# Kernel tuning notes

Measured on AMD Instinct MI355X. Metric: run time of the kernel, lower is better.

The kernel has to match this reference:

```python
import jax, jax.numpy as jnp
import numpy as np

B, N, D, H = 2, 2048, 512, 8
HD = D // H
EPS = 1e-5


def layernorm(x, g, b):
    m = jnp.mean(x, axis=-1, keepdims=True)
    v = jnp.var(x, axis=-1, keepdims=True)
    return (x - m) * jax.lax.rsqrt(v + EPS) * g + b


def setup_inputs() -> dict:
    key = jax.random.key(0)
    ks = jax.random.split(key, 16)
    s = 1.0 / np.sqrt(D)
    def lin(k, din, dout):
        k1, k2 = jax.random.split(k)
        return (jax.random.uniform(k1, (din, dout), jnp.float32, -s, s),
                jax.random.uniform(k2, (dout,), jnp.float32, -s, s))
    Wq, bq = lin(ks[0], D, D)
    Wk, bk = lin(ks[1], D, D)
    Wv, bv = lin(ks[2], D, D)
    Wo, bo = lin(ks[3], D, D)
    W1, b1 = lin(ks[4], D, 2 * D)
    W2, b2 = lin(ks[5], 2 * D, D)
    return {
        'y': jax.random.normal(ks[6], (B, N, D), jnp.float32),
        'Wq': Wq, 'bq': bq, 'Wk': Wk, 'bk': bk, 'Wv': Wv, 'bv': bv,
        'Wo': Wo, 'bo': bo,
        'ln1_g': jnp.ones((D,)), 'ln1_b': jnp.zeros((D,)),
        'ln2_g': jnp.ones((D,)), 'ln2_b': jnp.zeros((D,)),
        'W1': W1, 'b1': b1, 'W2': W2, 'b2': b2,
    }


def reference(y, Wq, bq, Wk, bk, Wv, bv, Wo, bo, ln1_g, ln1_b, ln2_g, ln2_b, W1, b1, W2, b2):
    x = layernorm(y, ln1_g, ln1_b)
    def heads(W, b):
        return (x @ W + b).reshape(B, N, H, HD).transpose(0, 2, 1, 3)  # bhnc
    q = heads(Wq, bq)
    k = heads(Wk, bk)
    v = heads(Wv, bv)
    score = jax.nn.softmax(jnp.einsum('bhic,bhjc->bhij', q, k) / np.sqrt(HD), axis=-1)
    r = jnp.einsum('bhij,bhjc->bhic', score, v)
    r = r.transpose(0, 2, 1, 3).reshape(B, N, D) @ Wo + bo
    y = y + r
    h = layernorm(y, ln2_g, ln2_b)
    h = jax.nn.gelu(h @ W1 + b1, approximate=False) @ W2 + b2
    return y + h
```

## Files before the change

kernel.cpp:

```cpp
#include <hip/hip_runtime.h>

#define DEVI __device__ __forceinline__

typedef unsigned short u16;
typedef unsigned int   u32;
typedef unsigned long long u64;
typedef float  f32x4  __attribute__((ext_vector_type(4)));
typedef __bf16 bf16x8 __attribute__((ext_vector_type(8)));

union FragU { bf16x8 b; u64 u[2]; __bf16 e[8]; };

DEVI u16 f2b(float x) { __bf16 t = (__bf16)x; return __builtin_bit_cast(u16, t); }

DEVI float exp2a(float x) { float r; asm("v_exp_f32 %0, %1" : "=v"(r) : "v"(x)); return r; }

DEVI void gload16(const void* g, void* l) {
  __builtin_amdgcn_global_load_lds((const __attribute__((address_space(1))) u32*)g,
                                   (__attribute__((address_space(3))) u32*)l, 16, 0, 0);
}

DEVI int kperm(int b) {
  return (b & 0x47) | ((b & 0x18) << 1) | ((b & 0x20) >> 2);
}
DEVI int swzo(int row, int b) {
  const int p = kperm(b);
  return ((((p >> 4) ^ row) & 7) << 4) | (p & 15);
}
DEVI FragU ldfrag(const char* base, int row, int g) {
  return *reinterpret_cast<const FragU*>(base + row * 128 + (((g ^ (row & 7)) << 4)));
}
DEVI size_t gaddr(int row, int kbyte, int rowbytes) {
  return (size_t)row * rowbytes + (size_t)((kbyte & ~127) + swzo(row, kbyte & 127));
}

__global__ __launch_bounds__(256)
void prep(const float* __restrict__ Wq, const float* __restrict__ Wk,
          const float* __restrict__ Wv, const float* __restrict__ Wo,
          const float* __restrict__ W1, const float* __restrict__ W2,
          u16* __restrict__ wqkvT, u16* __restrict__ woT,
          u16* __restrict__ w1T, u16* __restrict__ w2T,
          const float* __restrict__ y, const float* __restrict__ ln1g,
          const float* __restrict__ ln1b, char* __restrict__ xb) {
  const int id = blockIdx.x;
  if (id < 2048) {
    __shared__ float tile[32][33];
    const float* src; u16* dst; int K, N, bx, by;
    if (id < 1024) {
      const int m = id >> 8, t = id & 255;
      K = 512; N = 512; bx = t & 15; by = t >> 4;
      src = (m == 0) ? Wq : (m == 1) ? Wk : (m == 2) ? Wv : Wo;
      dst = (m == 3) ? woT : wqkvT + m * 512 * 512;
    } else if (id < 1536) {
      const int t = id - 1024; K = 512; N = 1024; bx = t & 31; by = t >> 5;
      src = W1; dst = w1T;
    } else {
      const int t = id - 1536; K = 1024; N = 512; bx = t & 15; by = t >> 4;
      src = W2; dst = w2T;
    }
    const int tx = threadIdx.x & 31, ty = threadIdx.x >> 5;
#pragma unroll
    for (int i = 0; i < 4; ++i)
      tile[ty + i * 8][tx] = src[(size_t)(by * 32 + ty + i * 8) * N + bx * 32 + tx];
    __syncthreads();
    const int nl = threadIdx.x >> 3, kq = threadIdx.x & 7;
    const int n = bx * 32 + nl;
    const int kg = by * 32 + kq * 4;
    union { ushort4 s; u64 q; } pk;
    pk.s.x = f2b(tile[kq * 4 + 0][nl]);
    pk.s.y = f2b(tile[kq * 4 + 1][nl]);
    pk.s.z = f2b(tile[kq * 4 + 2][nl]);
    pk.s.w = f2b(tile[kq * 4 + 3][nl]);
    *(u64*)((char*)dst + gaddr(n, 2 * kg, 2 * K)) = pk.q;
  } else {
    const int row = id - 2048;
    const int t = threadIdx.x;
    const float2 v = ((const float2*)(y + (size_t)row * 512))[t];
    float s1 = v.x + v.y, s2 = v.x * v.x + v.y * v.y;
#pragma unroll
    for (int off = 32; off; off >>= 1) { s1 += __shfl_xor(s1, off); s2 += __shfl_xor(s2, off); }
    __shared__ float a1[4], a2[4];
    const int w = t >> 6;
    if ((t & 63) == 0) { a1[w] = s1; a2[w] = s2; }
    __syncthreads();
    s1 = a1[0] + a1[1] + a1[2] + a1[3];
    s2 = a2[0] + a2[1] + a2[2] + a2[3];
    const float mean = s1 * (1.f / 512.f);
    const float var = s2 * (1.f / 512.f) - mean * mean;
    const float rstd = rsqrtf(var + 1e-5f);
    const float2 gg = ((const float2*)ln1g)[t];
    const float2 bb = ((const float2*)ln1b)[t];
    const u16 o0 = f2b((v.x - mean) * rstd * gg.x + bb.x);
    const u16 o1 = f2b((v.y - mean) * rstd * gg.y + bb.y);
    *(u32*)(xb + gaddr(row, 4 * t, 1024)) = (u32)o0 | ((u32)o1 << 16);
  }
}

__global__ __launch_bounds__(256)
void ln_bf16(const float* __restrict__ x, const float* __restrict__ g,
             const float* __restrict__ b, char* __restrict__ out) {
  const int row = blockIdx.x;
  const int t = threadIdx.x;
  const float2 v = ((const float2*)(x + (size_t)row * 512))[t];
  float s1 = v.x + v.y, s2 = v.x * v.x + v.y * v.y;
#pragma unroll
  for (int off = 32; off; off >>= 1) { s1 += __shfl_xor(s1, off); s2 += __shfl_xor(s2, off); }
  __shared__ float a1[4], a2[4];
  const int w = t >> 6;
  if ((t & 63) == 0) { a1[w] = s1; a2[w] = s2; }
  __syncthreads();
  s1 = a1[0] + a1[1] + a1[2] + a1[3];
  s2 = a2[0] + a2[1] + a2[2] + a2[3];
  const float mean = s1 * (1.f / 512.f);
  const float var = s2 * (1.f / 512.f) - mean * mean;
  const float rstd = rsqrtf(var + 1e-5f);
  const float2 gg = ((const float2*)g)[t];
  const float2 bb = ((const float2*)b)[t];
  const u16 o0 = f2b((v.x - mean) * rstd * gg.x + bb.x);
  const u16 o1 = f2b((v.y - mean) * rstd * gg.y + bb.y);
  *(u32*)(out + gaddr(row, 4 * t, 1024)) = (u32)o0 | ((u32)o1 << 16);
}

enum { EPI_QKV = 0, EPI_RES = 1, EPI_GELU = 2 };

template <int EPI, int WM, int WN, int AM, int AN>
__global__ __launch_bounds__(WM * WN * 64)
void gemm_bf16(const char* __restrict__ A, const char* __restrict__ Bt, int N, int K,
               const float* __restrict__ bias,
               const float* __restrict__ bq, const float* __restrict__ bk,
               const float* __restrict__ bv,
               const float* __restrict__ res, float* __restrict__ outF,
               char* __restrict__ outB,
               u16* __restrict__ qo, char* __restrict__ ko, char* __restrict__ vo) {
  constexpr int NW = WM * WN;
  constexpr int TM = WM * AM * 16, TN = WN * AN * 16;
  constexpr int NCHA = TM / 8, NCHB = TN / 8, NCH = NCHA + NCHB;
  constexpr int CPW = NCH / NW;
  static_assert(CPW * NW == NCH, "chunk split");
  __shared__ __align__(16) char sA[2][TM * 128];
  __shared__ __align__(16) char sB[2][TN * 128];
  const int tid = threadIdx.x;
  const int l = tid & 63, w = tid >> 6;
  const int tm = blockIdx.x, tn = blockIdx.y;
  const int wr = w / WN, wc = w % WN;
  const int u = l >> 4, r16 = l & 15;
  const int lrow = l >> 3, lgr = l & 7;
  f32x4 acc[AM][AN] = {};
  const size_t KB = (size_t)K * 2;
  const char* Ab = A + (size_t)(tm * TM) * KB;
  const char* Bb = Bt + (size_t)(tn * TN) * KB;
  const int nkt = K >> 6;
  auto stage = [&](int buf, int kt) {
#pragma unroll
    for (int i = 0; i < CPW; ++i) {
      const int c = w * CPW + i;
      if (c < NCHA) {
        gload16(Ab + (size_t)(c * 8 + lrow) * KB + (size_t)kt * 128 + (lgr << 4),
                sA[buf] + c * 1024);
      } else {
        const int c2 = c - NCHA;
        gload16(Bb + (size_t)(c2 * 8 + lrow) * KB + (size_t)kt * 128 + (lgr << 4),
                sB[buf] + c2 * 1024);
      }
    }
  };
  stage(0, 0);
  int cur = 0;
  for (int kt = 0; kt < nkt; ++kt) {
    __syncthreads();
    if (kt + 1 < nkt) stage(cur ^ 1, kt + 1);
    __builtin_amdgcn_s_setprio(1);
#pragma unroll
    for (int ks = 0; ks < 2; ++ks) {
      FragU af[AM], bfr[AN];
      const int g = ks * 4 + u;
#pragma unroll
      for (int i = 0; i < AM; ++i)
        af[i] = ldfrag(sA[cur], wr * (AM * 16) + i * 16 + r16, g);
#pragma unroll
      for (int i = 0; i < AN; ++i)
        bfr[i] = ldfrag(sB[cur], wc * (AN * 16) + i * 16 + r16, g);
#pragma unroll
      for (int mi = 0; mi < AM; ++mi)
#pragma unroll
        for (int ni = 0; ni < AN; ++ni)
          acc[mi][ni] = __builtin_amdgcn_mfma_f32_16x16x32_bf16(af[mi].b, bfr[ni].b,
                                                                acc[mi][ni], 0, 0, 0);
    }
    __builtin_amdgcn_s_setprio(0);
    cur ^= 1;
  }
  const int row0 = tm * TM + wr * (AM * 16) + (u << 2);
  const int col0 = tn * TN + wc * (AN * 16) + r16;
#pragma unroll
  for (int mi = 0; mi < AM; ++mi) {
#pragma unroll
    for (int ni = 0; ni < AN; ++ni) {
      const int col = col0 + ni * 16;
      if (EPI == EPI_RES) {
#pragma unroll
        for (int r = 0; r < 4; ++r) {
          const int row = row0 + mi * 16 + r;
          outF[(size_t)row * N + col] = acc[mi][ni][r] + bias[col] + res[(size_t)row * N + col];
        }
      } else if (EPI == EPI_GELU) {
#pragma unroll
        for (int r = 0; r < 4; ++r) {
          const int row = row0 + mi * 16 + r;
          const float x = acc[mi][ni][r] + bias[col];
          *(u16*)(outB + gaddr(row, 2 * col, 2 * N)) =
              f2b(0.5f * x * (1.f + erff(x * 0.70710678118f)));
        }
      } else {
        const int which = col >> 9, cc = col & 511;
        const int h = cc >> 6, hd = cc & 63;
        if (which == 2) {
          const int rowa = row0 + mi * 16;
          const int bb2 = rowa >> 11, nt0 = rowa & 2047;
          const int bh = bb2 * 8 + h;
          const float bvv = bv[cc];
          union { ushort4 s; u64 q; } pk;
          pk.s.x = f2b(acc[mi][ni][0] + bvv);
          pk.s.y = f2b(acc[mi][ni][1] + bvv);
          pk.s.z = f2b(acc[mi][ni][2] + bvv);
          pk.s.w = f2b(acc[mi][ni][3] + bvv);
          *(u64*)(vo + (size_t)bh * 262144 + (size_t)(nt0 >> 6) * 8192 +
                  gaddr(hd, 2 * (nt0 & 63), 128)) = pk.q;
        } else {
#pragma unroll
          for (int r = 0; r < 4; ++r) {
            const int row = row0 + mi * 16 + r;
            const int bb2 = row >> 11, nt = row & 2047;
            const int bh = bb2 * 8 + h;
            if (which == 0)
              qo[((size_t)bh * 2048 + nt) * 64 + hd] = f2b((acc[mi][ni][r] + bq[cc]) * 0.18033688f);
            else
              *(u16*)(ko + (size_t)bh * 262144 + (size_t)(nt >> 6) * 8192 +
                      gaddr(nt & 63, 2 * hd, 128)) = f2b(acc[mi][ni][r] + bk[cc]);
          }
        }
      }
    }
  }
}

__global__ __launch_bounds__(256)
void attn_k(const u16* __restrict__ q, const char* __restrict__ kswz,
            const char* __restrict__ vswz, char* __restrict__ r_out) {
  __shared__ __align__(16) char sK[2][2][8192];
  __shared__ __align__(16) char sV[2][2][8192];
  const int tid = threadIdx.x;
  const int l = tid & 63, w = tid >> 6;
  const int kvh = w & 1, qw = w >> 1;
  const int bh = blockIdx.x, qt = blockIdx.y;
  const int u = l >> 4, r16 = l & 15;
  const char* kp = kswz + (size_t)bh * 262144;
  const char* vp = vswz + (size_t)bh * 262144;
  auto stage = [&](int buf, int t) {
#pragma unroll
    for (int c = 0; c < 4; ++c) {
      gload16(kp + (size_t)t * 8192 + qw * 4096 + c * 1024 + l * 16,
              sK[kvh][buf] + qw * 4096 + c * 1024);
      gload16(vp + (size_t)t * 8192 + qw * 4096 + c * 1024 + l * 16,
              sV[kvh][buf] + qw * 4096 + c * 1024);
    }
  };
  stage(0, kvh * 16);
  FragU qf[2][2], ones;
  {
#pragma unroll
    for (int f = 0; f < 2; ++f) {
      const u16* qr = q + (size_t)bh * (2048 * 64) +
                      (size_t)(qt * 64 + qw * 32 + f * 16 + r16) * 64 + (u << 2);
      qf[f][0].u[0] = *(const u64*)qr;        qf[f][0].u[1] = *(const u64*)(qr + 16);
      qf[f][1].u[0] = *(const u64*)(qr + 32); qf[f][1].u[1] = *(const u64*)(qr + 48);
    }
    ones.u[0] = 0x3F803F803F803F80ull;
    ones.u[1] = 0x3F803F803F803F80ull;
  }
  f32x4 o[4][2] = {};
  f32x4 lacc[2] = {};
  int cur = 0;
  for (int i = 0; i < 16; ++i) {
    __syncthreads();
    if (i < 15) stage(cur ^ 1, kvh * 16 + i + 1);
    f32x4 st[4][2] = {};
    __builtin_amdgcn_s_setprio(1);
#pragma unroll
    for (int ks = 0; ks < 2; ++ks) {
      const int g = ks * 4 + u;
#pragma unroll
      for (int mi = 0; mi < 4; ++mi) {
        const FragU kf = ldfrag(sK[kvh][cur], mi * 16 + r16, g);
#pragma unroll
        for (int f = 0; f < 2; ++f)
          st[mi][f] = __builtin_amdgcn_mfma_f32_16x16x32_bf16(kf.b, qf[f][ks].b,
                                                              st[mi][f], 0, 0, 0);
      }
    }
    __builtin_amdgcn_s_setprio(0);
#pragma unroll
    for (int mi = 0; mi < 4; ++mi)
#pragma unroll
      for (int f = 0; f < 2; ++f)
#pragma unroll
        for (int r = 0; r < 4; ++r) st[mi][f][r] = exp2a(st[mi][f][r]);
    FragU pb[2][2];
#pragma unroll
    for (int f = 0; f < 2; ++f)
#pragma unroll
      for (int ks = 0; ks < 2; ++ks)
#pragma unroll
        for (int j = 0; j < 4; ++j) {
          pb[f][ks].e[j]     = (__bf16)st[2 * ks][f][j];
          pb[f][ks].e[j + 4] = (__bf16)st[2 * ks + 1][f][j];
        }
    __builtin_amdgcn_s_setprio(1);
#pragma unroll
    for (int ks = 0; ks < 2; ++ks) {
      const int g = ks * 4 + u;
#pragma unroll
      for (int f = 0; f < 2; ++f)
        lacc[f] = __builtin_amdgcn_mfma_f32_16x16x32_bf16(ones.b, pb[f][ks].b, lacc[f], 0, 0, 0);
#pragma unroll
      for (int mo = 0; mo < 4; ++mo) {
        const FragU vf = ldfrag(sV[kvh][cur], mo * 16 + r16, g);
#pragma unroll
        for (int f = 0; f < 2; ++f)
          o[mo][f] = __builtin_amdgcn_mfma_f32_16x16x32_bf16(vf.b, pb[f][ks].b,
                                                             o[mo][f], 0, 0, 0);
      }
    }
    __builtin_amdgcn_s_setprio(0);
    cur ^= 1;
  }
  __syncthreads();
  float* scrO = (float*)&sK[0][0][0];
  float* scrL = (float*)&sV[0][0][0];
  if (kvh == 1) {
    if (u == 0)
#pragma unroll
      for (int f = 0; f < 2; ++f) scrL[qw * 32 + f * 16 + r16] = lacc[f][0];
#pragma unroll
    for (int mo = 0; mo < 4; ++mo)
#pragma unroll
      for (int f = 0; f < 2; ++f)
#pragma unroll
        for (int r = 0; r < 4; ++r)
          scrO[qw * 2048 + (mo * 16 + u * 4 + r) * 32 + f * 16 + r16] = o[mo][f][r];
  }
  __syncthreads();
  if (kvh == 0) {
    const int h = bh & 7;
#pragma unroll
    for (int f = 0; f < 2; ++f) {
      const float linv = 1.f / (lacc[f][0] + scrL[qw * 32 + f * 16 + r16]);
      const int tok = (bh >> 3) * 2048 + qt * 64 + qw * 32 + f * 16 + r16;
#pragma unroll
      for (int mo = 0; mo < 4; ++mo) {
        union { ushort4 s; u64 qq; } pk;
        float vv[4];
#pragma unroll
        for (int r = 0; r < 4; ++r)
          vv[r] = (o[mo][f][r] + scrO[qw * 2048 + (mo * 16 + u * 4 + r) * 32 + f * 16 + r16]) * linv;
        pk.s.x = f2b(vv[0]); pk.s.y = f2b(vv[1]); pk.s.z = f2b(vv[2]); pk.s.w = f2b(vv[3]);
        *(u64*)(r_out + (size_t)tok * 1024 + h * 128 + swzo(tok, mo * 32 + (u << 3))) = pk.qq;
      }
    }
  }
}

extern "C" void kernel_launch(void* const* d_in, const int* in_sizes, int n_in,
                              void* d_out, int out_size, void* d_ws, size_t ws_size,
                              hipStream_t stream) {
  const float* y    = (const float*)d_in[0];
  const float* Wq   = (const float*)d_in[1];
  const float* bq   = (const float*)d_in[2];
  const float* Wk   = (const float*)d_in[3];
  const float* bk   = (const float*)d_in[4];
  const float* Wv   = (const float*)d_in[5];
  const float* bv   = (const float*)d_in[6];
  const float* Wo   = (const float*)d_in[7];
  const float* bo   = (const float*)d_in[8];
  const float* ln1g = (const float*)d_in[9];
  const float* ln1b = (const float*)d_in[10];
  const float* ln2g = (const float*)d_in[11];
  const float* ln2b = (const float*)d_in[12];
  const float* W1   = (const float*)d_in[13];
  const float* b1   = (const float*)d_in[14];
  const float* W2   = (const float*)d_in[15];
  const float* b2   = (const float*)d_in[16];
  float* out = (float*)d_out;
  char* ws = (char*)d_ws;
  char* xb    = ws;
  u16*  qb    = (u16*)(ws + (4u << 20));
  char* kswz  = ws + (8u << 20);
  char* vswz  = ws + (12u << 20);
  char* rb    = ws + (16u << 20);
  char* g1b   = ws + (20u << 20);
  u16* wqkvT  = (u16*)(ws + (28u << 20));
  u16* woT    = wqkvT + 1536 * 512;
  u16* w1T    = woT + 512 * 512;
  u16* w2T    = w1T + 1024 * 512;

  prep<<<6144, 256, 0, stream>>>(Wq, Wk, Wv, Wo, W1, W2, wqkvT, woT, w1T, w2T,
                                 y, ln1g, ln1b, xb);
  gemm_bf16<EPI_QKV, 2, 2, 4, 2><<<dim3(32, 24), 256, 0, stream>>>(
      xb, (const char*)wqkvT, 1536, 512, nullptr, bq, bk, bv,
      nullptr, nullptr, nullptr, qb, kswz, vswz);
  attn_k<<<dim3(16, 32), 256, 0, stream>>>(qb, kswz, vswz, rb);
  gemm_bf16<EPI_RES, 2, 2, 2, 2><<<dim3(64, 8), 256, 0, stream>>>(
      rb, (const char*)woT, 512, 512, bo, nullptr, nullptr, nullptr,
      y, out, nullptr, nullptr, nullptr, nullptr);
  ln_bf16<<<4096, 256, 0, stream>>>(out, ln2g, ln2b, xb);
  gemm_bf16<EPI_GELU, 2, 2, 4, 4><<<dim3(32, 8), 256, 0, stream>>>(
      xb, (const char*)w1T, 1024, 512, b1, nullptr, nullptr, nullptr,
      nullptr, nullptr, g1b, nullptr, nullptr, nullptr);
  gemm_bf16<EPI_RES, 2, 2, 2, 2><<<dim3(64, 8), 256, 0, stream>>>(
      g1b, (const char*)w2T, 512, 1024, b2, nullptr, nullptr, nullptr,
      out, out, nullptr, nullptr, nullptr, nullptr);
}
```

Before: 98.40 us.

## Split attention KV sequence four ways across 512-thread blocks with 32-key tiles

```diff
diff --git a/kernel.cpp b/kernel.cpp
--- a/kernel.cpp
+++ b/kernel.cpp
@@ -28,6 +28,9 @@
 }
 DEVI FragU ldfrag(const char* base, int row, int g) {
   return *reinterpret_cast<const FragU*>(base + row * 128 + (((g ^ (row & 7)) << 4)));
+}
+DEVI FragU ldfrag64(const char* base, int row, int g) {
+  return *reinterpret_cast<const FragU*>(base + row * 64 + (((g ^ (row & 3)) << 4)));
 }
 DEVI size_t gaddr(int row, int kbyte, int rowbytes) {
   return (size_t)row * rowbytes + (size_t)((kbyte & ~127) + swzo(row, kbyte & 127));
@@ -223,8 +226,9 @@
           pk.s.y = f2b(acc[mi][ni][1] + bvv);
           pk.s.z = f2b(acc[mi][ni][2] + bvv);
           pk.s.w = f2b(acc[mi][ni][3] + bvv);
-          *(u64*)(vo + (size_t)bh * 262144 + (size_t)(nt0 >> 6) * 8192 +
-                  gaddr(hd, 2 * (nt0 & 63), 128)) = pk.q;
+          const int kl = nt0 & 31;
+          const int off64 = ((((kl >> 2) & 3) ^ (hd & 3)) << 4) | (((kl >> 4) & 1) << 3);
+          *(u64*)(vo + (size_t)bh * 262144 + (size_t)(nt0 >> 5) * 4096 + hd * 64 + off64) = pk.q;
         } else {
 #pragma unroll
           for (int r = 0; r < 4; ++r) {
@@ -243,28 +247,30 @@
   }
 }
 
-__global__ __launch_bounds__(256)
+__global__ __launch_bounds__(512, 4)
 void attn_k(const u16* __restrict__ q, const char* __restrict__ kswz,
             const char* __restrict__ vswz, char* __restrict__ r_out) {
-  __shared__ __align__(16) char sK[2][2][8192];
-  __shared__ __align__(16) char sV[2][2][8192];
+  __shared__ __align__(16) char smem[65536];
+  char (*sK)[2][4096] = (char(*)[2][4096])smem;
+  char (*sV)[2][4096] = (char(*)[2][4096])(smem + 32768);
   const int tid = threadIdx.x;
   const int l = tid & 63, w = tid >> 6;
-  const int kvh = w & 1, qw = w >> 1;
+  const int kvh = w & 3, qw = w >> 2;
   const int bh = blockIdx.x, qt = blockIdx.y;
   const int u = l >> 4, r16 = l & 15;
   const char* kp = kswz + (size_t)bh * 262144;
   const char* vp = vswz + (size_t)bh * 262144;
-  auto stage = [&](int buf, int t) {
-#pragma unroll
-    for (int c = 0; c < 4; ++c) {
-      gload16(kp + (size_t)t * 8192 + qw * 4096 + c * 1024 + l * 16,
-              sK[kvh][buf] + qw * 4096 + c * 1024);
-      gload16(vp + (size_t)t * 8192 + qw * 4096 + c * 1024 + l * 16,
-              sV[kvh][buf] + qw * 4096 + c * 1024);
+  auto stage = [&](int buf, int i) {
+    const int t32 = kvh * 16 + i;
+    const size_t koff = (size_t)(t32 >> 1) * 8192 + (size_t)(t32 & 1) * 4096;
+    const size_t voff = (size_t)t32 * 4096;
+#pragma unroll
+    for (int c = 0; c < 2; ++c) {
+      gload16(kp + koff + qw * 2048 + c * 1024 + l * 16, sK[kvh][buf] + qw * 2048 + c * 1024);
+      gload16(vp + voff + qw * 2048 + c * 1024 + l * 16, sV[kvh][buf] + qw * 2048 + c * 1024);
     }
   };
-  stage(0, kvh * 16);
+  stage(0, 0);
   FragU qf[2][2], ones;
   {
 #pragma unroll
@@ -282,14 +288,14 @@
   int cur = 0;
   for (int i = 0; i < 16; ++i) {
     __syncthreads();
-    if (i < 15) stage(cur ^ 1, kvh * 16 + i + 1);
-    f32x4 st[4][2] = {};
+    if (i < 15) stage(cur ^ 1, i + 1);
+    f32x4 st[2][2] = {};
     __builtin_amdgcn_s_setprio(1);
 #pragma unroll
     for (int ks = 0; ks < 2; ++ks) {
       const int g = ks * 4 + u;
 #pragma unroll
-      for (int mi = 0; mi < 4; ++mi) {
+      for (int mi = 0; mi < 2; ++mi) {
         const FragU kf = ldfrag(sK[kvh][cur], mi * 16 + r16, g);
 #pragma unroll
         for (int f = 0; f < 2; ++f)
@@ -299,69 +305,73 @@
     }
     __builtin_amdgcn_s_setprio(0);
 #pragma unroll
-    for (int mi = 0; mi < 4; ++mi)
+    for (int mi = 0; mi < 2; ++mi)
 #pragma unroll
       for (int f = 0; f < 2; ++f)
 #pragma unroll
         for (int r = 0; r < 4; ++r) st[mi][f][r] = exp2a(st[mi][f][r]);
-    FragU pb[2][2];
+    FragU pb[2];
 #pragma unroll
     for (int f = 0; f < 2; ++f)
 #pragma unroll
-      for (int ks = 0; ks < 2; ++ks)
-#pragma unroll
-        for (int j = 0; j < 4; ++j) {
-          pb[f][ks].e[j]     = (__bf16)st[2 * ks][f][j];
-          pb[f][ks].e[j + 4] = (__bf16)st[2 * ks + 1][f][j];
-        }
+      for (int j = 0; j < 4; ++j) {
+        pb[f].e[j]     = (__bf16)st[0][f][j];
+        pb[f].e[j + 4] = (__bf16)st[1][f][j];
+      }
     __builtin_amdgcn_s_setprio(1);
 #pragma unroll
-    for (int ks = 0; ks < 2; ++ks) {
-      const int g = ks * 4 + u;
+    for (int f = 0; f < 2; ++f)
+      lacc[f] = __builtin_amdgcn_mfma_f32_16x16x32_bf16(ones.b, pb[f].b, lacc[f], 0, 0, 0);
+#pragma unroll
+    for (int mo = 0; mo < 4; ++mo) {
+      const FragU vf = ldfrag64(sV[kvh][cur], mo * 16 + r16, u);
 #pragma unroll
       for (int f = 0; f < 2; ++f)
-        lacc[f] = __builtin_amdgcn_mfma_f32_16x16x32_bf16(ones.b, pb[f][ks].b, lacc[f], 0, 0, 0);
-#pragma unroll
-      for (int mo = 0; mo < 4; ++mo) {
-        const FragU vf = ldfrag(sV[kvh][cur], mo * 16 + r16, g);
-#pragma unroll
-        for (int f = 0; f < 2; ++f)
-          o[mo][f] = __builtin_amdgcn_mfma_f32_16x16x32_bf16(vf.b, pb[f][ks].b,
-                                                             o[mo][f], 0, 0, 0);
-      }
+        o[mo][f] = __builtin_amdgcn_mfma_f32_16x16x32_bf16(vf.b, pb[f].b, o[mo][f], 0, 0, 0);
     }
     __builtin_amdgcn_s_setprio(0);
     cur ^= 1;
   }
   __syncthreads();
-  float* scrO = (float*)&sK[0][0][0];
-  float* scrL = (float*)&sV[0][0][0];
-  if (kvh == 1) {
+  float* scrO = (float*)smem;
+  float* scrL = (float*)smem + 12288;
+  if (kvh != 0) {
+    const int base = ((kvh - 1) * 2 + qw) * 2048;
     if (u == 0)
 #pragma unroll
-      for (int f = 0; f < 2; ++f) scrL[qw * 32 + f * 16 + r16] = lacc[f][0];
+      for (int f = 0; f < 2; ++f)
+        scrL[((kvh - 1) * 2 + qw) * 32 + f * 16 + r16] = lacc[f][0];
 #pragma unroll
     for (int mo = 0; mo < 4; ++mo)
 #pragma unroll
       for (int f = 0; f < 2; ++f)
 #pragma unroll
         for (int r = 0; r < 4; ++r)
-          scrO[qw * 2048 + (mo * 16 + u * 4 + r) * 32 + f * 16 + r16] = o[mo][f][r];
+          scrO[base + (mo * 16 + u * 4 + r) * 32 + f * 16 + r16] = o[mo][f][r];
   }
   __syncthreads();
   if (kvh == 0) {
     const int h = bh & 7;
 #pragma unroll
     for (int f = 0; f < 2; ++f) {
-      const float linv = 1.f / (lacc[f][0] + scrL[qw * 32 + f * 16 + r16]);
+      float lsum = lacc[f][0];
+#pragma unroll
+      for (int g2 = 0; g2 < 3; ++g2)
+        lsum += scrL[(g2 * 2 + qw) * 32 + f * 16 + r16];
+      const float linv = 1.f / lsum;
       const int tok = (bh >> 3) * 2048 + qt * 64 + qw * 32 + f * 16 + r16;
 #pragma unroll
       for (int mo = 0; mo < 4; ++mo) {
         union { ushort4 s; u64 qq; } pk;
         float vv[4];
 #pragma unroll
-        for (int r = 0; r < 4; ++r)
-          vv[r] = (o[mo][f][r] + scrO[qw * 2048 + (mo * 16 + u * 4 + r) * 32 + f * 16 + r16]) * linv;
+        for (int r = 0; r < 4; ++r) {
+          float acc2 = o[mo][f][r];
+#pragma unroll
+          for (int g2 = 0; g2 < 3; ++g2)
+            acc2 += scrO[(g2 * 2 + qw) * 2048 + (mo * 16 + u * 4 + r) * 32 + f * 16 + r16];
+          vv[r] = acc2 * linv;
+        }
         pk.s.x = f2b(vv[0]); pk.s.y = f2b(vv[1]); pk.s.z = f2b(vv[2]); pk.s.w = f2b(vv[3]);
         *(u64*)(r_out + (size_t)tok * 1024 + h * 128 + swzo(tok, mo * 32 + (u << 3))) = pk.qq;
       }
@@ -407,12 +417,12 @@
   gemm_bf16<EPI_QKV, 2, 2, 4, 2><<<dim3(32, 24), 256, 0, stream>>>(
       xb, (const char*)wqkvT, 1536, 512, nullptr, bq, bk, bv,
       nullptr, nullptr, nullptr, qb, kswz, vswz);
-  attn_k<<<dim3(16, 32), 256, 0, stream>>>(qb, kswz, vswz, rb);
+  attn_k<<<dim3(16, 32), 512, 0, stream>>>(qb, kswz, vswz, rb);
   gemm_bf16<EPI_RES, 2, 2, 2, 2><<<dim3(64, 8), 256, 0, stream>>>(
       rb, (const char*)woT, 512, 512, bo, nullptr, nullptr, nullptr,
       y, out, nullptr, nullptr, nullptr, nullptr);
   ln_bf16<<<4096, 256, 0, stream>>>(out, ln2g, ln2b, xb);
-  gemm_bf16<EPI_GELU, 2, 2, 4, 4><<<dim3(32, 8), 256, 0, stream>>>(
+  gemm_bf16<EPI_GELU, 2, 2, 4, 2><<<dim3(32, 16), 256, 0, stream>>>(
       xb, (const char*)w1T, 1024, 512, b1, nullptr, nullptr, nullptr,
       nullptr, nullptr, g1b, nullptr, nullptr, nullptr);
   gemm_bf16<EPI_RES, 2, 2, 2, 2><<<dim3(64, 8), 256, 0, stream>>>(
```

After: 90.68 us (median of 2 runs). -7.9%, faster.
